# Optimization experiments

Measured on AMD Instinct MI355X. Metric: run time of the kernel, lower is better.

The kernel has to match this reference:

```python
import jax, jax.numpy as jnp
import numpy as np


def setup_inputs() -> dict:
    key = jax.random.key(0)
    k1, k2, k3 = jax.random.split(key, 3)
    B, H, W, Cin, Cout = 8, 256, 256, 8, 8
    Fh, Fw = 2 * H - 1, 2 * W - 1  # SAME padding, unit strides -> kernel size 2k-1
    inputs = jax.random.normal(k1, (B, H, W, Cin), dtype=jnp.float32)
    # Kernel is parameterized directly in Fourier space; leading axis 2 = (real, imag).
    kernel = jax.random.normal(k2, (2, Fh, Fw, Cin, Cout), dtype=jnp.float32) * 0.01
    bias = jax.random.normal(k3, (Cout,), dtype=jnp.float32) * 0.01
    return {"inputs": inputs, "kernel": kernel, "bias": bias}


def reference(inputs, kernel, bias):
    # inputs: (B, H, W, Cin); kernel: (2, 2H-1, 2W-1, Cin, Cout); bias: (Cout,)
    B, H, W, Cin = inputs.shape
    Fh, Fw = 2 * H - 1, 2 * W - 1
    complex_kernel = jax.lax.complex(kernel[0], kernel[1])  # (Fh, Fw, Cin, Cout)
    # Zero-pad spatial dims to (2H-1, 2W-1) and FFT (s= pads at the end, same as jnp.pad).
    xf = jnp.fft.fftn(inputs, s=(Fh, Fw), axes=(1, 2))  # (B, Fh, Fw, Cin) complex
    # Contract over in_features in frequency space (linearity of IFFT makes this
    # mathematically identical to ifft-then-sum of the original, but avoids the
    # huge (B, Fh, Fw, Cin, Cout) intermediate).
    yf = jnp.einsum("bhwi,hwio->bhwo", xf, complex_kernel)
    y = jnp.fft.ifftn(yf, axes=(1, 2)).real  # (B, Fh, Fw, Cout)
    # SAME crop: centered slice of size (H, W).
    sh = (Fh - H) // 2
    sw = (Fw - W) // 2
    y = y[:, sh:sh + H, sw:sw + W, :]
    return y + bias
```

## Files before the change

kernel.cpp:

```cpp
#include <hip/hip_runtime.h>

#define TPB 256


typedef _Float16 half8  __attribute__((ext_vector_type(8)));
typedef float    floatx16 __attribute__((ext_vector_type(16)));
typedef unsigned int uintx4 __attribute__((ext_vector_type(4)));

__device__ __forceinline__ void split16(float v, _Float16& h, _Float16& l) {
    h = (_Float16)v;
    l = (_Float16)(v - (float)h);
}

__global__ __launch_bounds__(TPB)
void build_tables_k(_Float16* __restrict__ At, _Float16* __restrict__ Ct,
                    _Float16* __restrict__ C2) {
    int idx = blockIdx.x * TPB + threadIdx.x;
    const float w = (float)(6.28318530717958647692 / 511.0);
    _Float16* T; int R, kc2, K; int mode;
    if (idx < 16384)      { T = At; R = idx >> 5;  kc2 = idx & 31; K = 256; mode = 0; }
    else if (idx < 32768) { int id = idx - 16384; T = Ct; R = id >> 6; kc2 = id & 63; K = 512; mode = 1; }
    else                  { int id = idx - 32768; T = C2; R = id >> 5; kc2 = id & 31; K = 256; mode = 2; }

    half8 vrh, vrl, vih, vil;
    #pragma unroll
    for (int j = 0; j < 8; j++) {
        int k = kc2 * 8 + j;
        float cr = 0.f, ci = 0.f;
        if (mode == 0) {
            if (R < 511) {
                int m = (R * k) % 511;
                float s, c; sincosf(w * (float)m, &s, &c);
                cr = c; ci = -s;
            }
        } else {
            if (!(mode == 1 && k == 511)) {
                int m = (k * (R + 127)) % 511;
                float s, c; sincosf(w * (float)m, &s, &c);
                cr = c; ci = s;
            }
        }
        _Float16 th, tl;
        split16(cr, th, tl); vrh[j] = th; vrl[j] = tl;
        split16(ci, th, tl); vih[j] = th; vil[j] = tl;
    }
    int tile = R >> 5, kcblk = kc2 >> 1, lane = (R & 31) + 32 * (kc2 & 1);
    size_t base = ((size_t)(tile * (K >> 4) + kcblk) * 4) * 512 + lane * 8;
    *(half8*)(T + base)        = vrh;
    *(half8*)(T + base + 512)  = vrl;
    *(half8*)(T + base + 1024) = vih;
    *(half8*)(T + base + 1536) = vil;
}

__global__ __launch_bounds__(TPB)
void txp_k(const float* __restrict__ x, _Float16* __restrict__ xT) {
    __shared__ _Float16 L[8][2][32][40];
    const int tid = threadIdx.x;
    const int b = blockIdx.z, n0 = blockIdx.y * 32, w0 = blockIdx.x * 32;
    #pragma unroll
    for (int pp = 0; pp < 4; pp++) {
        int w = tid & 31, n = pp * 8 + (tid >> 5);
        const float4* src = (const float4*)(x + ((size_t)((b * 256 + n0 + n) * 256) + w0 + w) * 8);
        float4 v0 = src[0], v1 = src[1];
        float vv[8] = {v0.x, v0.y, v0.z, v0.w, v1.x, v1.y, v1.z, v1.w};
        #pragma unroll
        for (int ch = 0; ch < 8; ch++) {
            _Float16 h, lo; split16(vv[ch], h, lo);
            L[ch][0][w][n] = h;
            L[ch][1][w][n] = lo;
        }
    }
    __syncthreads();
    #pragma unroll
    for (int t = 0; t < 8; t++) {
        int c = tid + t * 256;
        int p = c & 1, cc = (c >> 1) & 3, w = (c >> 3) & 31, ch = c >> 8;
        uintx4 v = *(const uintx4*)&L[ch][p][w][cc * 8];
        size_t off = ((size_t)(b * 8 + ch)) * 131072 + (size_t)(w0 + w) * 512
                   + (size_t)((n0 >> 3) + cc) * 16 + p * 8;
        *(uintx4*)(xT + off) = v;
    }
}

__global__ __launch_bounds__(TPB)
void ksym_k(const float* __restrict__ Kr, const float* __restrict__ Ki,
            float* __restrict__ KeR, float* __restrict__ KeI) {
    __shared__ float LR[64][65];
    __shared__ float LI[64][65];
    const int tid = threadIdx.x;
    const int k2  = blockIdx.x >> 3;
    const int k1g = (blockIdx.x & 7) * 64;
    const int k2m = (k2 == 0) ? 0 : 511 - k2;
    const float sc = (k2 == 0) ? 0.5f : 1.0f;
    #pragma unroll
    for (int t = 0; t < 4; t++) {
        int idx = tid + t * 256;
        int j = idx & 15, k1l = idx >> 4;
        int k1 = k1g + k1l;
        float4 rs = {0,0,0,0}, rm = {0,0,0,0}, is = {0,0,0,0}, im = {0,0,0,0};
        if (k1 < 511) {
            int k1m = (k1 == 0) ? 0 : 511 - k1;
            size_t so = ((size_t)(k1  * 511 + k2 )) * 64 + j * 4;
            size_t mo = ((size_t)(k1m * 511 + k2m)) * 64 + j * 4;
            rs = *(const float4*)(Kr + so);
            rm = *(const float4*)(Kr + mo);
            is = *(const float4*)(Ki + so);
            im = *(const float4*)(Ki + mo);
        }
        LR[j*4+0][k1l] = sc * (rs.x + rm.x);
        LR[j*4+1][k1l] = sc * (rs.y + rm.y);
        LR[j*4+2][k1l] = sc * (rs.z + rm.z);
        LR[j*4+3][k1l] = sc * (rs.w + rm.w);
        LI[j*4+0][k1l] = sc * (is.x - im.x);
        LI[j*4+1][k1l] = sc * (is.y - im.y);
        LI[j*4+2][k1l] = sc * (is.z - im.z);
        LI[j*4+3][k1l] = sc * (is.w - im.w);
    }
    __syncthreads();
    const size_t ob = (size_t)k2 * 512 + k1g;
    #pragma unroll
    for (int t = 0; t < 4; t++) {
        int idx = tid + t * 256;
        int io = idx >> 4, fq = idx & 15;
        float4 vr = make_float4(LR[io][fq*4], LR[io][fq*4+1], LR[io][fq*4+2], LR[io][fq*4+3]);
        float4 vi = make_float4(LI[io][fq*4], LI[io][fq*4+1], LI[io][fq*4+2], LI[io][fq*4+3]);
        *(float4*)(KeR + (size_t)io * 131072 + ob + fq * 4) = vr;
        *(float4*)(KeI + (size_t)io * 131072 + ob + fq * 4) = vi;
    }
}

template<int NPD, bool TBA, bool DREAL>
__global__ __launch_bounds__(TPB, 2)
void mgemm_k(int K, const _Float16* __restrict__ Tf,
             const _Float16* __restrict__ Dd, long sDz,
             _Float16* __restrict__ Out, long sOz, int OutKc,
             float* __restrict__ Of, long sOfz, int OfN)
{
    constexpr int SLOTS = NPD * 2;
    constexpr int CPT   = NPD;
    __shared__ _Float16 sm[128 * SLOTS * 8];

    const int tid = threadIdx.x;
    const int bm = blockIdx.y * 128, bn = blockIdx.x * 128;
    const int z = blockIdx.z;
    const _Float16* D = Dd + (size_t)z * sDz;

    const int l  = tid & 63;
    const int wv = tid >> 6;
    const int lr = l & 31, lg = l >> 5;
    const int wm = (wv >> 1) * 64, wn = (wv & 1) * 64;
    const int Kc16 = K >> 4;

    const int tb = (TBA ? bm + wm : bn + wn);
    int tTB[2];
    #pragma unroll
    for (int t = 0; t < 2; t++) tTB[t] = ((tb + t * 32) >> 5) * Kc16;

    const int db = (TBA ? wn : wm);
    int dOff[2][NPD];
    #pragma unroll
    for (int t = 0; t < 2; t++) {
        int cl = db + t * 32 + lr;
        int sw = cl & (SLOTS - 1);
        #pragma unroll
        for (int p = 0; p < NPD; p++)
            dOff[t][p] = cl * (NPD * 16) + (((p * 2 + lg) ^ sw) * 8);
    }

    const int bSide = (TBA ? bn : bm);
    const _Float16* gP[CPT];
    int lO[CPT];
    #pragma unroll
    for (int j = 0; j < CPT; j++) {
        int cid = tid + j * TPB;
        int col = cid / SLOTS;
        int inner = cid & (SLOTS - 1);
        int p = inner & (NPD - 1);
        int h = inner / NPD;
        gP[j] = D + ((size_t)(bSide + col) * (K >> 3) + h) * (NPD * 8) + p * 8;
        lO[j] = col * (NPD * 16) + (((p * 2 + h) ^ (col & (SLOTS - 1))) * 8);
    }

    floatx16 accR[2][2], accI[2][2];
    #pragma unroll
    for (int i = 0; i < 2; i++)
        #pragma unroll
        for (int j = 0; j < 2; j++)
            #pragma unroll
            for (int r = 0; r < 16; r++) { accR[i][j][r] = 0.f; accI[i][j][r] = 0.f; }

    uintx4 st[CPT];
    #pragma unroll
    for (int j = 0; j < CPT; j++) { st[j] = *(const uintx4*)gP[j]; gP[j] += NPD * 16; }

    for (int k0 = 0; k0 < K; k0 += 16) {
        #pragma unroll
        for (int j = 0; j < CPT; j++) *(uintx4*)(sm + lO[j]) = st[j];
        __syncthreads();
        if (k0 + 16 < K) {
            #pragma unroll
            for (int j = 0; j < CPT; j++) { st[j] = *(const uintx4*)gP[j]; gP[j] += NPD * 16; }
        }

        const int kc0 = k0 >> 4;
        half8 tf[2][4];
        #pragma unroll
        for (int t = 0; t < 2; t++)
            #pragma unroll
            for (int p = 0; p < 4; p++)
                tf[t][p] = *(const half8*)(Tf + ((size_t)(tTB[t] + kc0) * 4 + p) * 512 + l * 8);
        half8 df[2][NPD];
        #pragma unroll
        for (int t = 0; t < 2; t++)
            #pragma unroll
            for (int p = 0; p < NPD; p++)
                df[t][p] = *(const half8*)(sm + dOff[t][p]);

        if constexpr (TBA && NPD == 4 && !DREAL) {
            half8 na[2][2];
            #pragma unroll
            for (int t = 0; t < 2; t++)
                #pragma unroll
                for (int p = 0; p < 2; p++) {
                    uintx4 u = __builtin_bit_cast(uintx4, tf[t][2 + p]);
                    u ^= 0x80008000u;
                    na[t][p] = __builtin_bit_cast(half8, u);
                }
            #pragma unroll
            for (int nt = 0; nt < 2; nt++)
                #pragma unroll
                for (int mt = 0; mt < 2; mt++) {
                    accR[mt][nt] = __builtin_amdgcn_mfma_f32_32x32x16_f16(tf[mt][0], df[nt][0], accR[mt][nt], 0,0,0);
                    accR[mt][nt] = __builtin_amdgcn_mfma_f32_32x32x16_f16(tf[mt][0], df[nt][1], accR[mt][nt], 0,0,0);
                    accR[mt][nt] = __builtin_amdgcn_mfma_f32_32x32x16_f16(tf[mt][1], df[nt][0], accR[mt][nt], 0,0,0);
                    accR[mt][nt] = __builtin_amdgcn_mfma_f32_32x32x16_f16(na[mt][0], df[nt][2], accR[mt][nt], 0,0,0);
                    accR[mt][nt] = __builtin_amdgcn_mfma_f32_32x32x16_f16(na[mt][0], df[nt][3], accR[mt][nt], 0,0,0);
                    accR[mt][nt] = __builtin_amdgcn_mfma_f32_32x32x16_f16(na[mt][1], df[nt][2], accR[mt][nt], 0,0,0);
                    accI[mt][nt] = __builtin_amdgcn_mfma_f32_32x32x16_f16(tf[mt][0], df[nt][2], accI[mt][nt], 0,0,0);
                    accI[mt][nt] = __builtin_amdgcn_mfma_f32_32x32x16_f16(tf[mt][0], df[nt][3], accI[mt][nt], 0,0,0);
                    accI[mt][nt] = __builtin_amdgcn_mfma_f32_32x32x16_f16(tf[mt][1], df[nt][2], accI[mt][nt], 0,0,0);
                    accI[mt][nt] = __builtin_amdgcn_mfma_f32_32x32x16_f16(tf[mt][2], df[nt][0], accI[mt][nt], 0,0,0);
                    accI[mt][nt] = __builtin_amdgcn_mfma_f32_32x32x16_f16(tf[mt][2], df[nt][1], accI[mt][nt], 0,0,0);
                    accI[mt][nt] = __builtin_amdgcn_mfma_f32_32x32x16_f16(tf[mt][3], df[nt][0], accI[mt][nt], 0,0,0);
                }
        } else if constexpr (TBA && NPD == 2) {
            #pragma unroll
            for (int nt = 0; nt < 2; nt++)
                #pragma unroll
                for (int mt = 0; mt < 2; mt++) {
                    accR[mt][nt] = __builtin_amdgcn_mfma_f32_32x32x16_f16(tf[mt][0], df[nt][0], accR[mt][nt], 0,0,0);
                    accR[mt][nt] = __builtin_amdgcn_mfma_f32_32x32x16_f16(tf[mt][0], df[nt][1], accR[mt][nt], 0,0,0);
                    accR[mt][nt] = __builtin_amdgcn_mfma_f32_32x32x16_f16(tf[mt][1], df[nt][0], accR[mt][nt], 0,0,0);
                    accI[mt][nt] = __builtin_amdgcn_mfma_f32_32x32x16_f16(tf[mt][2], df[nt][0], accI[mt][nt], 0,0,0);
                    accI[mt][nt] = __builtin_amdgcn_mfma_f32_32x32x16_f16(tf[mt][2], df[nt][1], accI[mt][nt], 0,0,0);
                    accI[mt][nt] = __builtin_amdgcn_mfma_f32_32x32x16_f16(tf[mt][3], df[nt][0], accI[mt][nt], 0,0,0);
                }
        } else {
            half8 na[2][2];
            #pragma unroll
            for (int t = 0; t < 2; t++)
                #pragma unroll
                for (int p = 0; p < 2; p++) {
                    uintx4 u = __builtin_bit_cast(uintx4, df[t][2 + p]);
                    u ^= 0x80008000u;
                    na[t][p] = __builtin_bit_cast(half8, u);
                }
            #pragma unroll
            for (int nt = 0; nt < 2; nt++)
                #pragma unroll
                for (int mt = 0; mt < 2; mt++) {
                    accR[mt][nt] = __builtin_amdgcn_mfma_f32_32x32x16_f16(df[mt][0], tf[nt][0], accR[mt][nt], 0,0,0);
                    accR[mt][nt] = __builtin_amdgcn_mfma_f32_32x32x16_f16(df[mt][0], tf[nt][1], accR[mt][nt], 0,0,0);
                    accR[mt][nt] = __builtin_amdgcn_mfma_f32_32x32x16_f16(df[mt][1], tf[nt][0], accR[mt][nt], 0,0,0);
                    accR[mt][nt] = __builtin_amdgcn_mfma_f32_32x32x16_f16(na[mt][0], tf[nt][2], accR[mt][nt], 0,0,0);
                    accR[mt][nt] = __builtin_amdgcn_mfma_f32_32x32x16_f16(na[mt][0], tf[nt][3], accR[mt][nt], 0,0,0);
                    accR[mt][nt] = __builtin_amdgcn_mfma_f32_32x32x16_f16(na[mt][1], tf[nt][2], accR[mt][nt], 0,0,0);
                }
        }
        __syncthreads();
    }

    if constexpr (DREAL) {
        float* Dv = Of + (size_t)z * sOfz;
        #pragma unroll
        for (int mt = 0; mt < 2; mt++)
            #pragma unroll
            for (int nt = 0; nt < 2; nt++)
                #pragma unroll
                for (int r = 0; r < 16; r++) {
                    int row = bm + wm + mt * 32 + (r & 3) + 8 * (r >> 2) + 4 * lg;
                    int col = bn + wn + nt * 32 + lr;
                    Dv[(size_t)row * OfN + col] = accR[mt][nt][r];
                }
    } else {
        _Float16* O = Out + (size_t)z * sOz;
        #pragma unroll
        for (int mt = 0; mt < 2; mt++)
            #pragma unroll
            for (int nt = 0; nt < 2; nt++)
                #pragma unroll
                for (int r = 0; r < 16; r++) {
                    int row = bm + wm + mt * 32 + (r & 3) + 8 * (r >> 2) + 4 * lg;
                    int col = bn + wn + nt * 32 + lr;
                    size_t base = ((size_t)row * OutKc + (col >> 3)) * 32 + (col & 7);
                    _Float16 h, lo;
                    split16(accR[mt][nt][r], h, lo);
                    O[base]      = h;
                    O[base + 8]  = lo;
                    split16(accI[mt][nt][r], h, lo);
                    O[base + 16] = h;
                    O[base + 24] = lo;
                }
    }
}

__global__ __launch_bounds__(TPB)
void einsum_k(_Float16* __restrict__ F, const float* __restrict__ KeR,
              const float* __restrict__ KeI, int g)
{
    const int pt = blockIdx.x * TPB + threadIdx.x;
    const int k2 = pt >> 9, k1 = pt & 511;
    const size_t fo = ((size_t)(k2 * 64 + (k1 >> 3))) * 32 + (k1 & 7);

    for (int b0 = 0; b0 < g; b0 += 4) {
        const int bt = (g - b0 < 4) ? (g - b0) : 4;
        float xr[4][8], xi[4][8];
        #pragma unroll
        for (int bb = 0; bb < 4; bb++) {
            if (bb >= bt) break;
            #pragma unroll
            for (int i = 0; i < 8; i++) {
                const _Float16* P = F + ((size_t)((b0 + bb) * 8 + i)) * 524288 + fo;
                xr[bb][i] = (float)P[0]  + (float)P[8];
                xi[bb][i] = (float)P[16] + (float)P[24];
            }
        }
        #pragma unroll
        for (int o = 0; o < 8; o++) {
            float ar[4] = {0.f,0.f,0.f,0.f}, ai[4] = {0.f,0.f,0.f,0.f};
            #pragma unroll
            for (int i = 0; i < 8; i++) {
                float kr = KeR[(size_t)(i * 8 + o) * 131072 + pt];
                float ki = KeI[(size_t)(i * 8 + o) * 131072 + pt];
                #pragma unroll
                for (int bb = 0; bb < 4; bb++) {
                    ar[bb] = fmaf(xr[bb][i], kr, ar[bb]);
                    ar[bb] = fmaf(-xi[bb][i], ki, ar[bb]);
                    ai[bb] = fmaf(xr[bb][i], ki, ai[bb]);
                    ai[bb] = fmaf(xi[bb][i], kr, ai[bb]);
                }
            }
            #pragma unroll
            for (int bb = 0; bb < 4; bb++) {
                if (bb >= bt) break;
                _Float16* Q = F + ((size_t)((b0 + bb) * 8 + o)) * 524288 + fo;
                _Float16 h, lo;
                split16(ar[bb], h, lo); Q[0]  = h; Q[8]  = lo;
                split16(ai[bb], h, lo); Q[16] = h; Q[24] = lo;
            }
        }
    }
}

__global__ __launch_bounds__(TPB)
void tout_k(const float* __restrict__ Dq, const float* __restrict__ bias,
            float* __restrict__ out, int b0)
{
    int idx = blockIdx.x * TPB + threadIdx.x;
    int o = idx & 7, q = (idx >> 3) & 255, p = (idx >> 11) & 255, bl = idx >> 19;
    float v = Dq[(size_t)(bl * 8 + o) * 65536 + p * 256 + q];
    out[(size_t)(b0 + bl) * 524288 + (size_t)(idx & 524287)] = v * (1.f / 261121.f) + bias[o];
}


extern "C" void kernel_launch(void* const* d_in, const int* in_sizes, int n_in,
                              void* d_out, int out_size, void* d_ws, size_t ws_size,
                              hipStream_t stream) {
    const float* x    = (const float*)d_in[0];
    const float* Kr   = (const float*)d_in[1];
    const float* Ki   = Kr + 16711744;
    const float* bias = (const float*)d_in[2];
    float* out = (float*)d_out;
    char* ws = (char*)d_ws;

    _Float16* AtabF = (_Float16*)(ws + 0);
    _Float16* CtabF = (_Float16*)(ws + 1048576);
    _Float16* Ct2F  = (_Float16*)(ws + 2097152);
    _Float16* xTp   = (_Float16*)(ws + 2621440);
    float*    KeR   = (float*)   (ws + 19398656);
    float*    KeI   = (float*)   (ws + 52953088);
    const size_t fixedEnd = 86507520;

    int g = 1;
    for (int cand = 8; cand >= 1; cand >>= 1) {
        if (fixedEnd + (size_t)cand * 16777216 <= ws_size) { g = cand; break; }
    }
    _Float16* F1  = (_Float16*)(ws + fixedEnd);
    _Float16* F2T = (_Float16*)(ws + fixedEnd + (size_t)g * 8388608);
    _Float16* F1b = F1;
    float*    Dq  = (float*)F2T;

    build_tables_k<<<160, TPB, 0, stream>>>(AtabF, CtabF, Ct2F);
    txp_k<<<dim3(8, 8, 8), TPB, 0, stream>>>(x, xTp);
    ksym_k<<<2048, TPB, 0, stream>>>(Kr, Ki, KeR, KeI);

    for (int b0 = 0; b0 < 8; b0 += g) {
        int Z = g * 8;
        mgemm_k<2, true, false><<<dim3(2, 4, Z), TPB, 0, stream>>>(
            256, AtabF,
            xTp + (size_t)b0 * 8 * 131072, 131072,
            F1, 524288, 32, nullptr, 0, 0);

        mgemm_k<4, true, false><<<dim3(4, 2, Z), TPB, 0, stream>>>(
            256, AtabF,
            F1, 524288,
            F2T, 524288, 64, nullptr, 0, 0);

        einsum_k<<<512, TPB, 0, stream>>>(F2T, KeR, KeI, g);

        mgemm_k<4, true, false><<<dim3(2, 2, Z), TPB, 0, stream>>>(
            512, CtabF,
            F2T, 524288,
            F1b, 262144, 32, nullptr, 0, 0);

        mgemm_k<4, false, true><<<dim3(2, 2, Z), TPB, 0, stream>>>(
            256, Ct2F,
            F1b, 262144,
            nullptr, 0, 0, Dq, 65536, 256);

        tout_k<<<g * 2048, TPB, 0, stream>>>(Dq, bias, out, b0);
    }
}
```

Before: 504.5 us.

## Halve GEMM N-tile, double-buffer LDS, and raise occupancy in mgemm_k

Shrinks the per-block tile on the data side from 128 to 64 columns and doubles the grid x-dimension. This gives more blocks to spread across the CUs, and `launch_bounds` now allows 3 blocks per SM. The shared-memory staging becomes a two-buffer ping-pong with one barrier per k-step instead of two, so the next tile is stored while the current one feeds the MFMAs. In exchange, each wave keeps fewer accumulators, and the twiddle-table fragments are fetched from global memory by more blocks, which adds redundant table traffic.

```diff
diff --git a/kernel.cpp b/kernel.cpp
--- a/kernel.cpp
+++ b/kernel.cpp
@@ -130,36 +130,40 @@
 }
 
 template<int NPD, bool TBA, bool DREAL>
-__global__ __launch_bounds__(TPB, 2)
+__global__ __launch_bounds__(TPB, 3)
 void mgemm_k(int K, const _Float16* __restrict__ Tf,
              const _Float16* __restrict__ Dd, long sDz,
              _Float16* __restrict__ Out, long sOz, int OutKc,
              float* __restrict__ Of, long sOfz, int OfN)
 {
     constexpr int SLOTS = NPD * 2;
-    constexpr int CPT   = NPD;
-    __shared__ _Float16 sm[128 * SLOTS * 8];
+    constexpr int DE  = TBA ? 64 : 128;
+    constexpr int DT  = TBA ? 1 : 2;
+    constexpr int TT  = TBA ? 2 : 1;
+    constexpr int CPT = DE * SLOTS / TPB;
+    constexpr int BUF = DE * SLOTS * 8;
+    __shared__ _Float16 sm[2 * BUF];
 
     const int tid = threadIdx.x;
-    const int bm = blockIdx.y * 128, bn = blockIdx.x * 128;
+    const int bm = blockIdx.y * 128, bn = blockIdx.x * 64;
     const int z = blockIdx.z;
     const _Float16* D = Dd + (size_t)z * sDz;
 
     const int l  = tid & 63;
     const int wv = tid >> 6;
     const int lr = l & 31, lg = l >> 5;
-    const int wm = (wv >> 1) * 64, wn = (wv & 1) * 64;
+    const int wm = (wv >> 1) * 64, wn = (wv & 1) * 32;
     const int Kc16 = K >> 4;
 
     const int tb = (TBA ? bm + wm : bn + wn);
-    int tTB[2];
-    #pragma unroll
-    for (int t = 0; t < 2; t++) tTB[t] = ((tb + t * 32) >> 5) * Kc16;
+    int tTB[TT];
+    #pragma unroll
+    for (int t = 0; t < TT; t++) tTB[t] = ((tb + t * 32) >> 5) * Kc16;
 
     const int db = (TBA ? wn : wm);
-    int dOff[2][NPD];
-    #pragma unroll
-    for (int t = 0; t < 2; t++) {
+    int dOff[DT][NPD];
+    #pragma unroll
+    for (int t = 0; t < DT; t++) {
         int cl = db + t * 32 + lr;
         int sw = cl & (SLOTS - 1);
         #pragma unroll
@@ -181,103 +185,105 @@
         lO[j] = col * (NPD * 16) + (((p * 2 + h) ^ (col & (SLOTS - 1))) * 8);
     }
 
-    floatx16 accR[2][2], accI[2][2];
+    floatx16 accR[2], accI[2];
     #pragma unroll
     for (int i = 0; i < 2; i++)
         #pragma unroll
-        for (int j = 0; j < 2; j++)
-            #pragma unroll
-            for (int r = 0; r < 16; r++) { accR[i][j][r] = 0.f; accI[i][j][r] = 0.f; }
+        for (int r = 0; r < 16; r++) { accR[i][r] = 0.f; accI[i][r] = 0.f; }
 
     uintx4 st[CPT];
     #pragma unroll
     for (int j = 0; j < CPT; j++) { st[j] = *(const uintx4*)gP[j]; gP[j] += NPD * 16; }
-
-    for (int k0 = 0; k0 < K; k0 += 16) {
-        #pragma unroll
-        for (int j = 0; j < CPT; j++) *(uintx4*)(sm + lO[j]) = st[j];
-        __syncthreads();
-        if (k0 + 16 < K) {
-            #pragma unroll
-            for (int j = 0; j < CPT; j++) { st[j] = *(const uintx4*)gP[j]; gP[j] += NPD * 16; }
-        }
-
-        const int kc0 = k0 >> 4;
-        half8 tf[2][4];
-        #pragma unroll
-        for (int t = 0; t < 2; t++)
+    #pragma unroll
+    for (int j = 0; j < CPT; j++) *(uintx4*)(sm + lO[j]) = st[j];
+    #pragma unroll
+    for (int j = 0; j < CPT; j++) { st[j] = *(const uintx4*)gP[j]; gP[j] += NPD * 16; }
+    __syncthreads();
+
+    const int NT = K >> 4;
+    for (int t = 0; t < NT; t++) {
+        const int cur = t & 1;
+        const _Float16* smc = sm + cur * BUF;
+
+        half8 tf[TT][4];
+        #pragma unroll
+        for (int tt = 0; tt < TT; tt++)
             #pragma unroll
             for (int p = 0; p < 4; p++)
-                tf[t][p] = *(const half8*)(Tf + ((size_t)(tTB[t] + kc0) * 4 + p) * 512 + l * 8);
-        half8 df[2][NPD];
-        #pragma unroll
-        for (int t = 0; t < 2; t++)
+                tf[tt][p] = *(const half8*)(Tf + ((size_t)(tTB[tt] + t) * 4 + p) * 512 + l * 8);
+        half8 df[DT][NPD];
+        #pragma unroll
+        for (int dt = 0; dt < DT; dt++)
             #pragma unroll
             for (int p = 0; p < NPD; p++)
-                df[t][p] = *(const half8*)(sm + dOff[t][p]);
+                df[dt][p] = *(const half8*)(smc + dOff[dt][p]);
 
         if constexpr (TBA && NPD == 4 && !DREAL) {
             half8 na[2][2];
             #pragma unroll
-            for (int t = 0; t < 2; t++)
+            for (int mt = 0; mt < 2; mt++)
                 #pragma unroll
                 for (int p = 0; p < 2; p++) {
-                    uintx4 u = __builtin_bit_cast(uintx4, tf[t][2 + p]);
+                    uintx4 u = __builtin_bit_cast(uintx4, tf[mt][2 + p]);
                     u ^= 0x80008000u;
-                    na[t][p] = __builtin_bit_cast(half8, u);
+                    na[mt][p] = __builtin_bit_cast(half8, u);
                 }
             #pragma unroll
-            for (int nt = 0; nt < 2; nt++)
-                #pragma unroll
-                for (int mt = 0; mt < 2; mt++) {
-                    accR[mt][nt] = __builtin_amdgcn_mfma_f32_32x32x16_f16(tf[mt][0], df[nt][0], accR[mt][nt], 0,0,0);
-                    accR[mt][nt] = __builtin_amdgcn_mfma_f32_32x32x16_f16(tf[mt][0], df[nt][1], accR[mt][nt], 0,0,0);
-                    accR[mt][nt] = __builtin_amdgcn_mfma_f32_32x32x16_f16(tf[mt][1], df[nt][0], accR[mt][nt], 0,0,0);
-                    accR[mt][nt] = __builtin_amdgcn_mfma_f32_32x32x16_f16(na[mt][0], df[nt][2], accR[mt][nt], 0,0,0);
-                    accR[mt][nt] = __builtin_amdgcn_mfma_f32_32x32x16_f16(na[mt][0], df[nt][3], accR[mt][nt], 0,0,0);
-                    accR[mt][nt] = __builtin_amdgcn_mfma_f32_32x32x16_f16(na[mt][1], df[nt][2], accR[mt][nt], 0,0,0);
-                    accI[mt][nt] = __builtin_amdgcn_mfma_f32_32x32x16_f16(tf[mt][0], df[nt][2], accI[mt][nt], 0,0,0);
-                    accI[mt][nt] = __builtin_amdgcn_mfma_f32_32x32x16_f16(tf[mt][0], df[nt][3], accI[mt][nt], 0,0,0);
-                    accI[mt][nt] = __builtin_amdgcn_mfma_f32_32x32x16_f16(tf[mt][1], df[nt][2], accI[mt][nt], 0,0,0);
-                    accI[mt][nt] = __builtin_amdgcn_mfma_f32_32x32x16_f16(tf[mt][2], df[nt][0], accI[mt][nt], 0,0,0);
-                    accI[mt][nt] = __builtin_amdgcn_mfma_f32_32x32x16_f16(tf[mt][2], df[nt][1], accI[mt][nt], 0,0,0);
-                    accI[mt][nt] = __builtin_amdgcn_mfma_f32_32x32x16_f16(tf[mt][3], df[nt][0], accI[mt][nt], 0,0,0);
-                }
+            for (int mt = 0; mt < 2; mt++) {
+                accR[mt] = __builtin_amdgcn_mfma_f32_32x32x16_f16(tf[mt][0], df[0][0], accR[mt], 0,0,0);
+                accR[mt] = __builtin_amdgcn_mfma_f32_32x32x16_f16(tf[mt][0], df[0][1], accR[mt], 0,0,0);
+                accR[mt] = __builtin_amdgcn_mfma_f32_32x32x16_f16(tf[mt][1], df[0][0], accR[mt], 0,0,0);
+                accR[mt] = __builtin_amdgcn_mfma_f32_32x32x16_f16(na[mt][0], df[0][2], accR[mt], 0,0,0);
+                accR[mt] = __builtin_amdgcn_mfma_f32_32x32x16_f16(na[mt][0], df[0][3], accR[mt], 0,0,0);
+                accR[mt] = __builtin_amdgcn_mfma_f32_32x32x16_f16(na[mt][1], df[0][2], accR[mt], 0,0,0);
+                accI[mt] = __builtin_amdgcn_mfma_f32_32x32x16_f16(tf[mt][0], df[0][2], accI[mt], 0,0,0);
+                accI[mt] = __builtin_amdgcn_mfma_f32_32x32x16_f16(tf[mt][0], df[0][3], accI[mt], 0,0,0);
+                accI[mt] = __builtin_amdgcn_mfma_f32_32x32x16_f16(tf[mt][1], df[0][2], accI[mt], 0,0,0);
+                accI[mt] = __builtin_amdgcn_mfma_f32_32x32x16_f16(tf[mt][2], df[0][0], accI[mt], 0,0,0);
+                accI[mt] = __builtin_amdgcn_mfma_f32_32x32x16_f16(tf[mt][2], df[0][1], accI[mt], 0,0,0);
+                accI[mt] = __builtin_amdgcn_mfma_f32_32x32x16_f16(tf[mt][3], df[0][0], accI[mt], 0,0,0);
+            }
         } else if constexpr (TBA && NPD == 2) {
             #pragma unroll
-            for (int nt = 0; nt < 2; nt++)
-                #pragma unroll
-                for (int mt = 0; mt < 2; mt++) {
-                    accR[mt][nt] = __builtin_amdgcn_mfma_f32_32x32x16_f16(tf[mt][0], df[nt][0], accR[mt][nt], 0,0,0);
-                    accR[mt][nt] = __builtin_amdgcn_mfma_f32_32x32x16_f16(tf[mt][0], df[nt][1], accR[mt][nt], 0,0,0);
-                    accR[mt][nt] = __builtin_amdgcn_mfma_f32_32x32x16_f16(tf[mt][1], df[nt][0], accR[mt][nt], 0,0,0);
-                    accI[mt][nt] = __builtin_amdgcn_mfma_f32_32x32x16_f16(tf[mt][2], df[nt][0], accI[mt][nt], 0,0,0);
-                    accI[mt][nt] = __builtin_amdgcn_mfma_f32_32x32x16_f16(tf[mt][2], df[nt][1], accI[mt][nt], 0,0,0);
-                    accI[mt][nt] = __builtin_amdgcn_mfma_f32_32x32x16_f16(tf[mt][3], df[nt][0], accI[mt][nt], 0,0,0);
-                }
+            for (int mt = 0; mt < 2; mt++) {
+                accR[mt] = __builtin_amdgcn_mfma_f32_32x32x16_f16(tf[mt][0], df[0][0], accR[mt], 0,0,0);
+                accR[mt] = __builtin_amdgcn_mfma_f32_32x32x16_f16(tf[mt][0], df[0][1], accR[mt], 0,0,0);
+                accR[mt] = __builtin_amdgcn_mfma_f32_32x32x16_f16(tf[mt][1], df[0][0], accR[mt], 0,0,0);
+                accI[mt] = __builtin_amdgcn_mfma_f32_32x32x16_f16(tf[mt][2], df[0][0], accI[mt], 0,0,0);
+                accI[mt] = __builtin_amdgcn_mfma_f32_32x32x16_f16(tf[mt][2], df[0][1], accI[mt], 0,0,0);
+                accI[mt] = __builtin_amdgcn_mfma_f32_32x32x16_f16(tf[mt][3], df[0][0], accI[mt], 0,0,0);
+            }
         } else {
-            half8 na[2][2];
-            #pragma unroll
-            for (int t = 0; t < 2; t++)
+            half8 nd[2][2];
+            #pragma unroll
+            for (int mt = 0; mt < 2; mt++)
                 #pragma unroll
                 for (int p = 0; p < 2; p++) {
-                    uintx4 u = __builtin_bit_cast(uintx4, df[t][2 + p]);
+                    uintx4 u = __builtin_bit_cast(uintx4, df[mt][2 + p]);
                     u ^= 0x80008000u;
-                    na[t][p] = __builtin_bit_cast(half8, u);
+                    nd[mt][p] = __builtin_bit_cast(half8, u);
                 }
             #pragma unroll
-            for (int nt = 0; nt < 2; nt++)
+            for (int mt = 0; mt < 2; mt++) {
+                accR[mt] = __builtin_amdgcn_mfma_f32_32x32x16_f16(df[mt][0], tf[0][0], accR[mt], 0,0,0);
+                accR[mt] = __builtin_amdgcn_mfma_f32_32x32x16_f16(df[mt][0], tf[0][1], accR[mt], 0,0,0);
+                accR[mt] = __builtin_amdgcn_mfma_f32_32x32x16_f16(df[mt][1], tf[0][0], accR[mt], 0,0,0);
+                accR[mt] = __builtin_amdgcn_mfma_f32_32x32x16_f16(nd[mt][0], tf[0][2], accR[mt], 0,0,0);
+                accR[mt] = __builtin_amdgcn_mfma_f32_32x32x16_f16(nd[mt][0], tf[0][3], accR[mt], 0,0,0);
+                accR[mt] = __builtin_amdgcn_mfma_f32_32x32x16_f16(nd[mt][1], tf[0][2], accR[mt], 0,0,0);
+            }
+        }
+
+        if (t + 1 < NT) {
+            _Float16* smn = sm + (cur ^ 1) * BUF;
+            #pragma unroll
+            for (int j = 0; j < CPT; j++) *(uintx4*)(smn + lO[j]) = st[j];
+            if (t + 2 < NT) {
                 #pragma unroll
-                for (int mt = 0; mt < 2; mt++) {
-                    accR[mt][nt] = __builtin_amdgcn_mfma_f32_32x32x16_f16(df[mt][0], tf[nt][0], accR[mt][nt], 0,0,0);
-                    accR[mt][nt] = __builtin_amdgcn_mfma_f32_32x32x16_f16(df[mt][0], tf[nt][1], accR[mt][nt], 0,0,0);
-                    accR[mt][nt] = __builtin_amdgcn_mfma_f32_32x32x16_f16(df[mt][1], tf[nt][0], accR[mt][nt], 0,0,0);
-                    accR[mt][nt] = __builtin_amdgcn_mfma_f32_32x32x16_f16(na[mt][0], tf[nt][2], accR[mt][nt], 0,0,0);
-                    accR[mt][nt] = __builtin_amdgcn_mfma_f32_32x32x16_f16(na[mt][0], tf[nt][3], accR[mt][nt], 0,0,0);
-                    accR[mt][nt] = __builtin_amdgcn_mfma_f32_32x32x16_f16(na[mt][1], tf[nt][2], accR[mt][nt], 0,0,0);
-                }
-        }
-        __syncthreads();
+                for (int j = 0; j < CPT; j++) { st[j] = *(const uintx4*)gP[j]; gP[j] += NPD * 16; }
+            }
+            __syncthreads();
+        }
     }
 
     if constexpr (DREAL) {
@@ -285,32 +291,28 @@
         #pragma unroll
         for (int mt = 0; mt < 2; mt++)
             #pragma unroll
-            for (int nt = 0; nt < 2; nt++)
-                #pragma unroll
-                for (int r = 0; r < 16; r++) {
-                    int row = bm + wm + mt * 32 + (r & 3) + 8 * (r >> 2) + 4 * lg;
-                    int col = bn + wn + nt * 32 + lr;
-                    Dv[(size_t)row * OfN + col] = accR[mt][nt][r];
-                }
+            for (int r = 0; r < 16; r++) {
+                int row = bm + wm + mt * 32 + (r & 3) + 8 * (r >> 2) + 4 * lg;
+                int col = bn + wn + lr;
+                Dv[(size_t)row * OfN + col] = accR[mt][r];
+            }
     } else {
         _Float16* O = Out + (size_t)z * sOz;
         #pragma unroll
         for (int mt = 0; mt < 2; mt++)
             #pragma unroll
-            for (int nt = 0; nt < 2; nt++)
-                #pragma unroll
-                for (int r = 0; r < 16; r++) {
-                    int row = bm + wm + mt * 32 + (r & 3) + 8 * (r >> 2) + 4 * lg;
-                    int col = bn + wn + nt * 32 + lr;
-                    size_t base = ((size_t)row * OutKc + (col >> 3)) * 32 + (col & 7);
-                    _Float16 h, lo;
-                    split16(accR[mt][nt][r], h, lo);
-                    O[base]      = h;
-                    O[base + 8]  = lo;
-                    split16(accI[mt][nt][r], h, lo);
-                    O[base + 16] = h;
-                    O[base + 24] = lo;
-                }
+            for (int r = 0; r < 16; r++) {
+                int row = bm + wm + mt * 32 + (r & 3) + 8 * (r >> 2) + 4 * lg;
+                int col = bn + wn + lr;
+                size_t base = ((size_t)row * OutKc + (col >> 3)) * 32 + (col & 7);
+                _Float16 h, lo;
+                split16(accR[mt][r], h, lo);
+                O[base]      = h;
+                O[base + 8]  = lo;
+                split16(accI[mt][r], h, lo);
+                O[base + 16] = h;
+                O[base + 24] = lo;
+            }
     }
 }
 
@@ -406,24 +408,24 @@
 
     for (int b0 = 0; b0 < 8; b0 += g) {
         int Z = g * 8;
-        mgemm_k<2, true, false><<<dim3(2, 4, Z), TPB, 0, stream>>>(
+        mgemm_k<2, true, false><<<dim3(4, 4, Z), TPB, 0, stream>>>(
             256, AtabF,
             xTp + (size_t)b0 * 8 * 131072, 131072,
             F1, 524288, 32, nullptr, 0, 0);
 
-        mgemm_k<4, true, false><<<dim3(4, 2, Z), TPB, 0, stream>>>(
+        mgemm_k<4, true, false><<<dim3(8, 2, Z), TPB, 0, stream>>>(
             256, AtabF,
             F1, 524288,
             F2T, 524288, 64, nullptr, 0, 0);
 
         einsum_k<<<512, TPB, 0, stream>>>(F2T, KeR, KeI, g);
 
-        mgemm_k<4, true, false><<<dim3(2, 2, Z), TPB, 0, stream>>>(
+        mgemm_k<4, true, false><<<dim3(4, 2, Z), TPB, 0, stream>>>(
             512, CtabF,
             F2T, 524288,
             F1b, 262144, 32, nullptr, 0, 0);
 
-        mgemm_k<4, false, true><<<dim3(2, 2, Z), TPB, 0, stream>>>(
+        mgemm_k<4, false, true><<<dim3(4, 2, Z), TPB, 0, stream>>>(
             256, Ct2F,
             F1b, 262144,
             nullptr, 0, 0, Dq, 65536, 256);
```

Measured after the change: 506.3 us. About the same (+0.4%).
